# Optimization experiments

Measured on AMD Instinct MI355X. Metric: run time of the kernel, lower is better.

Reference implementation:

```python
import jax, jax.numpy as jnp
import numpy as np

B, N, C = 4, 4096, 256
H, D, K = 8, 32, 16  # heads, dim_head, knn


def setup_inputs() -> dict:
    key = jax.random.key(0)
    ks = jax.random.split(key, 7)
    s = 1.0 / np.sqrt(C)
    return {
        "x": jax.random.normal(ks[0], (B, N, C), dtype=jnp.float32),
        "Wq": jax.random.normal(ks[1], (C, H * D), dtype=jnp.float32) * s,
        "bq": jnp.zeros((H * D,), dtype=jnp.float32),
        "Wk": jax.random.normal(ks[2], (C, H * D), dtype=jnp.float32) * s,
        "bk": jnp.zeros((H * D,), dtype=jnp.float32),
        "Wv": jax.random.normal(ks[3], (C, H * D), dtype=jnp.float32) * s,
        "bv": jnp.zeros((H * D,), dtype=jnp.float32),
    }


def _knn_indices(x):
    # squared euclidean distances per batch: [B, N, N]
    sq = jnp.sum(x * x, axis=-1)
    d2 = sq[:, :, None] + sq[:, None, :] - 2.0 * jnp.einsum("bnc,bmc->bnm", x, x)
    # exclude self-loops (loop=False)
    eye = jnp.eye(x.shape[1], dtype=bool)
    d2 = jnp.where(eye[None], jnp.inf, d2)
    # k nearest neighbors (smallest distance)
    _, idx = jax.lax.top_k(-d2, K)  # [B, N, K]
    return idx


def reference(x, Wq, bq, Wk, bk, Wv, bv):
    idx = _knn_indices(x)  # [B, N, K] neighbor (source) node ids per target node
    # gather neighbor features: [B, N, K, C]
    xj = jax.vmap(lambda xb, ib: xb[ib])(x, idx)
    q = (x @ Wq + bq).reshape(B, N, H, D)           # target-node queries
    ke = (xj @ Wk + bk).reshape(B, N, K, H, D)      # per-edge keys
    ve = (xj @ Wv + bv).reshape(B, N, K, H, D)      # per-edge values
    scale = 1.0 / np.sqrt(D)
    scores = jnp.einsum("bnhd,bnkhd->bnkh", q, ke) * scale
    alpha = jax.nn.softmax(scores, axis=2)          # softmax over each node's K neighbors
    out = jnp.einsum("bnkh,bnkhd->bnhd", alpha, ve)
    return out.reshape(B, N, H * D)
```

## Files before the change

kernel.cpp:

```cpp
#include <hip/hip_runtime.h>
#include <cstdint>
#include <cstddef>

#define N_ 4096
#define C_ 256

typedef _Float16 h8 __attribute__((ext_vector_type(8)));
typedef _Float16 h4 __attribute__((ext_vector_type(4)));
typedef float f4 __attribute__((ext_vector_type(4)));

__device__ __forceinline__ void gl2lds16(const void* g, void* l) {
  __builtin_amdgcn_global_load_lds((const __attribute__((address_space(1))) void*)g,
                                   (__attribute__((address_space(3))) void*)l, 16, 0, 0);
}

__device__ __forceinline__ void ce_asc(double& a, double& b) {
  double mn = fmin(a, b), mx = fmax(a, b);
  a = mn; b = mx;
}

__device__ __forceinline__ void sort8_asc(double* c) {
#pragma unroll
  for (int k = 2; k <= 8; k <<= 1)
#pragma unroll
    for (int j = k >> 1; j > 0; j >>= 1)
#pragma unroll
      for (int i = 0; i < 8; i++) {
        int l = i ^ j;
        if (l > i) {
          bool up = ((i & k) == 0);
          double a = c[i], b = c[l];
          double mn = fmin(a, b), mx = fmax(a, b);
          c[i] = up ? mn : mx;
          c[l] = up ? mx : mn;
        }
      }
}

__device__ __forceinline__ void merge8_top16(double* karr, const double* c) {
#pragma unroll
  for (int i = 0; i < 8; i++)
    karr[8 + i] = fmin(karr[8 + i], c[7 - i]);
#pragma unroll
  for (int j = 8; j > 0; j >>= 1)
#pragma unroll
    for (int i = 0; i < 16; i++) {
      int l = i ^ j;
      if (l > i) ce_asc(karr[i], karr[l]);
    }
}

__global__ __launch_bounds__(256) void k_prep(const float* __restrict__ x,
                                              float* __restrict__ sq,
                                              _Float16* __restrict__ xh,
                                              _Float16* __restrict__ xl) {
  int wave = threadIdx.x >> 6, lane = threadIdx.x & 63;
  int row = blockIdx.x * 4 + wave;
  size_t off = (size_t)row * C_ + lane * 4;
  float4 v = *(const float4*)(x + off);
  h4 hi; hi[0] = (_Float16)v.x; hi[1] = (_Float16)v.y;
         hi[2] = (_Float16)v.z; hi[3] = (_Float16)v.w;
  h4 lo; lo[0] = (_Float16)(v.x - (float)hi[0]); lo[1] = (_Float16)(v.y - (float)hi[1]);
         lo[2] = (_Float16)(v.z - (float)hi[2]); lo[3] = (_Float16)(v.w - (float)hi[3]);
  *(h4*)(xh + off) = hi;
  *(h4*)(xl + off) = lo;
  float s = v.x * v.x + v.y * v.y + v.z * v.z + v.w * v.w;
  s += __shfl_xor(s, 32); s += __shfl_xor(s, 16); s += __shfl_xor(s, 8);
  s += __shfl_xor(s, 4);  s += __shfl_xor(s, 2);  s += __shfl_xor(s, 1);
  if (lane == 0) sq[row] = s;
}

__global__ __launch_bounds__(256) void k_wsplit(const float* __restrict__ Wq,
                                                const float* __restrict__ Wk,
                                                const float* __restrict__ Wv,
                                                _Float16* __restrict__ wh,
                                                _Float16* __restrict__ wl) {
  int g = blockIdx.x * 256 + threadIdx.x;
  int m = g >> 16, e = g & 65535;
  int k = e >> 8, j = e & 255;
  const float* W = (m == 0) ? Wq : ((m == 1) ? Wk : Wv);
  float v = W[k * 256 + j];
  _Float16 hi = (_Float16)v;
  _Float16 lo = (_Float16)(v - (float)hi);
  wh[m * 65536 + j * 256 + k] = hi;
  wl[m * 65536 + j * 256 + k] = lo;
}

__global__ __launch_bounds__(256, 3) void k_proj(const _Float16* __restrict__ xh,
                                                 const _Float16* __restrict__ xl,
                                                 const _Float16* __restrict__ wh,
                                                 const _Float16* __restrict__ wl,
                                                 const float* __restrict__ bqp,
                                                 const float* __restrict__ bkp,
                                                 const float* __restrict__ bvp,
                                                 float* __restrict__ qf,
                                                 float* __restrict__ kf,
                                                 float* __restrict__ vf) {
  int tid = threadIdx.x;
  int bid = blockIdx.x;
  int m   = bid >> 8;
  int rb  = (bid >> 1) & 127;
  int cp  = bid & 1;
  int wave = tid >> 6, lane = tid & 63, quad = lane >> 4, l16 = lane & 15;
  const float* bb = (m == 0) ? bqp : ((m == 1) ? bkp : bvp);
  float* dst      = (m == 0) ? qf  : ((m == 1) ? kf  : vf);
  int row0 = rb * 128 + wave * 32;

  h8 Ah[2][8], Al[2][8];
#pragma unroll
  for (int rt = 0; rt < 2; rt++)
#pragma unroll
    for (int kc = 0; kc < 8; kc++) {
      size_t off = (size_t)(row0 + rt * 16 + l16) * C_ + kc * 32 + quad * 8;
      Ah[rt][kc] = *(const h8*)(xh + off);
      Al[rt][kc] = *(const h8*)(xl + off);
    }
  const _Float16* whm = wh + (size_t)m * 65536;
  const _Float16* wlm = wl + (size_t)m * 65536;

  f4 acc[2][8];
#pragma unroll
  for (int rt = 0; rt < 2; rt++)
#pragma unroll
    for (int ct = 0; ct < 8; ct++) acc[rt][ct] = f4{0.f, 0.f, 0.f, 0.f};
#pragma unroll
  for (int kc = 0; kc < 8; kc++) {
#pragma unroll
    for (int ct = 0; ct < 8; ct++) {
      int col = cp * 128 + ct * 16 + l16;
      h8 bh = *(const h8*)(whm + (size_t)col * 256 + kc * 32 + quad * 8);
      h8 bl = *(const h8*)(wlm + (size_t)col * 256 + kc * 32 + quad * 8);
#pragma unroll
      for (int rt = 0; rt < 2; rt++) {
        acc[rt][ct] = __builtin_amdgcn_mfma_f32_16x16x32_f16(Ah[rt][kc], bh, acc[rt][ct], 0, 0, 0);
        acc[rt][ct] = __builtin_amdgcn_mfma_f32_16x16x32_f16(Ah[rt][kc], bl, acc[rt][ct], 0, 0, 0);
        acc[rt][ct] = __builtin_amdgcn_mfma_f32_16x16x32_f16(Al[rt][kc], bh, acc[rt][ct], 0, 0, 0);
      }
    }
  }
#pragma unroll
  for (int rt = 0; rt < 2; rt++)
#pragma unroll
    for (int ct = 0; ct < 8; ct++) {
      int col = cp * 128 + ct * 16 + l16;
      float bias = bb[col];
#pragma unroll
      for (int i = 0; i < 4; i++) {
        int r = row0 + rt * 16 + quad * 4 + i;
        dst[(size_t)r * C_ + col] = acc[rt][ct][i] + bias;
      }
    }
}

__global__ __launch_bounds__(256, 2) void k_knn(const _Float16* __restrict__ xh,
                                                const _Float16* __restrict__ xl,
                                                const float* __restrict__ sq,
                                                double* __restrict__ pd) {
  __shared__ __align__(16) _Float16 Bh[16 * 528];
  __shared__ __align__(16) _Float16 Bl[16 * 528];
  __shared__ __align__(16) float sc[128 * 36];
  __shared__ float sqS[32];

  int tid = threadIdx.x;
  int wave = tid >> 6, lane = tid & 63, quad = lane >> 4, l16 = lane & 15;
  int bid = blockIdx.x;
  int s4 = bid & 3, tile = (bid >> 2) & 31, b = bid >> 7;
  int bN = b * N_, n0 = tile * 128, src0g = s4 * 1024;

  h8 Ah[2][8], Al[2][8];
  int tb = bN + n0 + wave * 32;
#pragma unroll
  for (int rt = 0; rt < 2; rt++)
#pragma unroll
    for (int kc = 0; kc < 8; kc++) {
      size_t off = (size_t)(tb + rt * 16 + l16) * C_ + kc * 32 + quad * 8;
      Ah[rt][kc] = *(const h8*)(xh + off);
      Al[rt][kc] = *(const h8*)(xl + off);
    }
  float sqT[2][4];
#pragma unroll
  for (int rt = 0; rt < 2; rt++)
#pragma unroll
    for (int i = 0; i < 4; i++)
      sqT[rt][i] = sq[tb + rt * 16 + quad * 4 + i];

  double karr[16];
#pragma unroll
  for (int p = 0; p < 16; p++) karr[p] = 1e300;
  int rowo = tid & 127, half = tid >> 7;

  {
    const _Float16* gh = xh + (size_t)(bN + src0g) * C_ + lane * 8;
    const _Float16* gl = xl + (size_t)(bN + src0g) * C_ + lane * 8;
#pragma unroll
    for (int k = 0; k < 4; k++) {
      int seg = wave * 4 + k;
      gl2lds16(gh + seg * 512, &Bh[seg * 528]);
      gl2lds16(gl + seg * 512, &Bl[seg * 528]);
    }
    if (tid < 32) sqS[tid] = sq[bN + src0g + tid];
  }

  int hb0 = ((l16 >> 1) * 528) + ((l16 & 1) * 256) + quad * 8;
  int hb1 = (((16 + l16) >> 1) * 528) + ((l16 & 1) * 256) + quad * 8;

#pragma unroll 1
  for (int ch = 0; ch < 32; ch++) {
    int src0 = src0g + ch * 32;
    __syncthreads();

    f4 acc[2][2];
#pragma unroll
    for (int rt = 0; rt < 2; rt++)
#pragma unroll
      for (int ct = 0; ct < 2; ct++) acc[rt][ct] = f4{0.f, 0.f, 0.f, 0.f};
#pragma unroll
    for (int kc = 0; kc < 8; kc++) {
      h8 bh0 = *(const h8*)(&Bh[hb0 + kc * 32]);
      h8 bh1 = *(const h8*)(&Bh[hb1 + kc * 32]);
      h8 bl0 = *(const h8*)(&Bl[hb0 + kc * 32]);
      h8 bl1 = *(const h8*)(&Bl[hb1 + kc * 32]);
#pragma unroll
      for (int rt = 0; rt < 2; rt++) {
        acc[rt][0] = __builtin_amdgcn_mfma_f32_16x16x32_f16(Ah[rt][kc], bh0, acc[rt][0], 0, 0, 0);
        acc[rt][0] = __builtin_amdgcn_mfma_f32_16x16x32_f16(Ah[rt][kc], bl0, acc[rt][0], 0, 0, 0);
        acc[rt][0] = __builtin_amdgcn_mfma_f32_16x16x32_f16(Al[rt][kc], bh0, acc[rt][0], 0, 0, 0);
        acc[rt][1] = __builtin_amdgcn_mfma_f32_16x16x32_f16(Ah[rt][kc], bh1, acc[rt][1], 0, 0, 0);
        acc[rt][1] = __builtin_amdgcn_mfma_f32_16x16x32_f16(Ah[rt][kc], bl1, acc[rt][1], 0, 0, 0);
        acc[rt][1] = __builtin_amdgcn_mfma_f32_16x16x32_f16(Al[rt][kc], bh1, acc[rt][1], 0, 0, 0);
      }
    }
    float sqSr[2] = {sqS[l16], sqS[16 + l16]};
#pragma unroll
    for (int rt = 0; rt < 2; rt++)
#pragma unroll
      for (int ct = 0; ct < 2; ct++) {
        int c = ct * 16 + l16;
#pragma unroll
        for (int i = 0; i < 4; i++) {
          int r = wave * 32 + rt * 16 + quad * 4 + i;
          float d2 = sqT[rt][i] + sqSr[ct] - 2.0f * acc[rt][ct][i];
          if (n0 + r == src0 + c) d2 = 1e38f;
          sc[r * 36 + c] = d2;
        }
      }
    __syncthreads();

    if (ch < 31) {
      int srcn = src0 + 32;
      const _Float16* gh = xh + (size_t)(bN + srcn) * C_ + lane * 8;
      const _Float16* gl = xl + (size_t)(bN + srcn) * C_ + lane * 8;
#pragma unroll
      for (int k = 0; k < 4; k++) {
        int seg = wave * 4 + k;
        gl2lds16(gh + seg * 512, &Bh[seg * 528]);
        gl2lds16(gl + seg * 512, &Bl[seg * 528]);
      }
      if (tid < 32) sqS[tid] = sq[bN + srcn + tid];
    }

#pragma unroll
    for (int bt = 0; bt < 2; bt++) {
      float dv[8];
#pragma unroll
      for (int k4 = 0; k4 < 2; k4++)
        *(float4*)&dv[k4 * 4] = *(const float4*)(&sc[rowo * 36 + half * 16 + bt * 8 + k4 * 4]);
      double c8[8];
#pragma unroll
      for (int j = 0; j < 8; j++) {
        double key = (double)dv[j];
        c8[j] = __longlong_as_double(__double_as_longlong(key) |
                                     (unsigned)(src0 + half * 16 + bt * 8 + j));
      }
      sort8_asc(c8);
      merge8_top16(karr, c8);
    }
  }

  __syncthreads();
  double* scd = (double*)sc;
  if (tid >= 128) {
#pragma unroll
    for (int p = 0; p < 16; p++) scd[(tid - 128) * 17 + p] = karr[p];
  }
  __syncthreads();
  if (tid < 128) {
#pragma unroll
    for (int i = 0; i < 16; i++)
      karr[i] = fmin(karr[i], scd[tid * 17 + (15 - i)]);
#pragma unroll
    for (int j = 8; j > 0; j >>= 1)
#pragma unroll
      for (int i = 0; i < 16; i++) {
        int l = i ^ j;
        if (l > i) ce_asc(karr[i], karr[l]);
      }
#pragma unroll
    for (int p = 0; p < 16; p++)
      pd[((size_t)bid * 128 + tid) * 16 + p] = karr[p];
  }
}

__global__ __launch_bounds__(256) void k_kmerge(const double* __restrict__ pd,
                                                int* __restrict__ idxo) {
  int g = blockIdx.x * 256 + threadIdx.x;
  int b = g >> 12, n = g & 4095;
  int tile = n >> 7, r = n & 127;
  size_t base[4]; int p[4]; double hd[4];
#pragma unroll
  for (int s = 0; s < 4; s++) {
    base[s] = (size_t)(((b * 32 + tile) * 4 + s) * 128 + r) * 16;
    p[s] = 0;
    hd[s] = pd[base[s]];
  }
#pragma unroll
  for (int k = 0; k < 16; k++) {
    int bs = 0; double bd = hd[0];
#pragma unroll
    for (int s = 1; s < 4; s++) if (hd[s] < bd) { bd = hd[s]; bs = s; }
    idxo[(size_t)g * 16 + k] = (int)(__double_as_longlong(bd) & 0xFFF);
    p[bs]++;
    hd[bs] = (p[bs] < 16) ? pd[base[bs] + p[bs]] : 1e301;
  }
}

__global__ __launch_bounds__(256) void k_attn(const float* __restrict__ qf,
                                              const float* __restrict__ kf,
                                              const float* __restrict__ vf,
                                              const int* __restrict__ idxv,
                                              float* __restrict__ out) {
  int wave = threadIdx.x >> 6, lane = threadIdx.x & 63;
  int g = blockIdx.x * 4 + wave;
  int bN = (g >> 12) << 12;
  float4 q4 = *(const float4*)(qf + (size_t)g * C_ + lane * 4);
  int my = idxv[(size_t)g * 16 + (lane & 15)];
  const float scale = 0.17677669529663687f;

  float s[16];
  float4 vv[16];
#pragma unroll
  for (int j = 0; j < 16; j++) {
    int nb = __shfl(my, j);
    size_t base = (size_t)(bN + nb) * C_ + lane * 4;
    float4 k4 = *(const float4*)(kf + base);
    vv[j] = *(const float4*)(vf + base);
    float p = k4.x * q4.x + k4.y * q4.y + k4.z * q4.z + k4.w * q4.w;
    p += __shfl_xor(p, 1); p += __shfl_xor(p, 2); p += __shfl_xor(p, 4);
    s[j] = p * scale;
  }
  float mx = s[0];
#pragma unroll
  for (int j = 1; j < 16; j++) mx = fmaxf(mx, s[j]);
  float den = 0.f;
#pragma unroll
  for (int j = 0; j < 16; j++) { s[j] = __expf(s[j] - mx); den += s[j]; }
  float inv = 1.0f / den;
  float4 o; o.x = 0.f; o.y = 0.f; o.z = 0.f; o.w = 0.f;
#pragma unroll
  for (int j = 0; j < 16; j++) {
    float w = s[j] * inv;
    o.x = fmaf(w, vv[j].x, o.x); o.y = fmaf(w, vv[j].y, o.y);
    o.z = fmaf(w, vv[j].z, o.z); o.w = fmaf(w, vv[j].w, o.w);
  }
  *(float4*)(out + (size_t)g * C_ + lane * 4) = o;
}

extern "C" void kernel_launch(void* const* d_in, const int* in_sizes, int n_in,
                              void* d_out, int out_size, void* d_ws, size_t ws_size,
                              hipStream_t stream) {
  const float* x  = (const float*)d_in[0];
  const float* Wq = (const float*)d_in[1];
  const float* bq = (const float*)d_in[2];
  const float* Wk = (const float*)d_in[3];
  const float* bk = (const float*)d_in[4];
  const float* Wv = (const float*)d_in[5];
  const float* bv = (const float*)d_in[6];
  float* out = (float*)d_out;

  char* ws = (char*)d_ws;
  float*     sqp  = (float*)(ws + 0);
  _Float16*  xh   = (_Float16*)(ws + 65536);
  _Float16*  xl   = (_Float16*)(ws + 8454144);
  float*     qf   = (float*)(ws + 16842752);
  float*     kf   = (float*)(ws + 33619968);
  float*     vf   = (float*)(ws + 50397184);
  double*    pd   = (double*)(ws + 67174400);
  int*       idxb = (int*)  (ws + 75563008);
  _Float16*  whf  = (_Float16*)(ws + 76611584);
  _Float16*  wlf  = (_Float16*)(ws + 77004800);

  k_prep  <<<4096, 256, 0, stream>>>(x, sqp, xh, xl);
  k_wsplit<<<768,  256, 0, stream>>>(Wq, Wk, Wv, whf, wlf);
  k_proj  <<<768,  256, 0, stream>>>(xh, xl, whf, wlf, bq, bk, bv, qf, kf, vf);
  k_knn   <<<512,  256, 0, stream>>>(xh, xl, sqp, pd);
  k_kmerge<<<64,   256, 0, stream>>>(pd, idxb);
  k_attn  <<<4096, 256, 0, stream>>>(qf, kf, vf, idxb, out);
}
```

Baseline: 294.9 us.

## Use float key/int index pairs in kNN top-k, bitonic merge in kmerge

The per-thread top-16 lists in the kNN kernel now keep float distances and int indices separately instead of packed doubles, so the comparators do 32-bit selects rather than double-precision min/max. The MFMA calls are reordered so the four independent accumulators interleave, which shortens back-to-back dependency chains. The final k-way merge kernel is replaced by a bitonic merge of four sorted 16-lists per thread and launched with smaller blocks to spread across more CUs. The cost is more registers for the separate index arrays and extra select instructions per swap.

```diff
diff --git a/kernel.cpp b/kernel.cpp
--- a/kernel.cpp
+++ b/kernel.cpp
@@ -14,39 +14,63 @@
                                    (__attribute__((address_space(3))) void*)l, 16, 0, 0);
 }
 
-__device__ __forceinline__ void ce_asc(double& a, double& b) {
-  double mn = fmin(a, b), mx = fmax(a, b);
-  a = mn; b = mx;
-}
-
-__device__ __forceinline__ void sort8_asc(double* c) {
-#pragma unroll
-  for (int k = 2; k <= 8; k <<= 1)
-#pragma unroll
-    for (int j = k >> 1; j > 0; j >>= 1)
+
+__device__ __forceinline__ void sort8p(float* k, int* x) {
+#pragma unroll
+  for (int kk = 2; kk <= 8; kk <<= 1)
+#pragma unroll
+    for (int j = kk >> 1; j > 0; j >>= 1)
 #pragma unroll
       for (int i = 0; i < 8; i++) {
         int l = i ^ j;
         if (l > i) {
-          bool up = ((i & k) == 0);
-          double a = c[i], b = c[l];
-          double mn = fmin(a, b), mx = fmax(a, b);
-          c[i] = up ? mn : mx;
-          c[l] = up ? mx : mn;
+          bool up = ((i & kk) == 0);
+          bool sw = up ? (k[i] > k[l]) : (k[i] < k[l]);
+          float a = sw ? k[l] : k[i];
+          float b = sw ? k[i] : k[l];
+          int ai = sw ? x[l] : x[i];
+          int bi = sw ? x[i] : x[l];
+          k[i] = a; k[l] = b; x[i] = ai; x[l] = bi;
         }
       }
 }
 
-__device__ __forceinline__ void merge8_top16(double* karr, const double* c) {
-#pragma unroll
-  for (int i = 0; i < 8; i++)
-    karr[8 + i] = fmin(karr[8 + i], c[7 - i]);
+__device__ __forceinline__ void merge8p(float* kk_, int* ki,
+                                        const float* ck, const int* ci) {
+#pragma unroll
+  for (int i = 0; i < 8; i++) {
+    bool take = ck[7 - i] < kk_[8 + i];
+    kk_[8 + i] = take ? ck[7 - i] : kk_[8 + i];
+    ki[8 + i]  = take ? ci[7 - i] : ki[8 + i];
+  }
 #pragma unroll
   for (int j = 8; j > 0; j >>= 1)
 #pragma unroll
     for (int i = 0; i < 16; i++) {
       int l = i ^ j;
-      if (l > i) ce_asc(karr[i], karr[l]);
+      if (l > i) {
+        bool sw = kk_[i] > kk_[l];
+        float a = sw ? kk_[l] : kk_[i];
+        float b = sw ? kk_[i] : kk_[l];
+        int ai = sw ? ki[l] : ki[i];
+        int bi = sw ? ki[i] : ki[l];
+        kk_[i] = a; kk_[l] = b; ki[i] = ai; ki[l] = bi;
+      }
+    }
+}
+
+__device__ __forceinline__ void merge16d(double* a, const double* b) {
+#pragma unroll
+  for (int i = 0; i < 16; i++) a[i] = fmin(a[i], b[15 - i]);
+#pragma unroll
+  for (int j = 8; j > 0; j >>= 1)
+#pragma unroll
+    for (int i = 0; i < 16; i++) {
+      int l = i ^ j;
+      if (l > i) {
+        double mn = fmin(a[i], a[l]), mx = fmax(a[i], a[l]);
+        a[i] = mn; a[l] = mx;
+      }
     }
 }
 
@@ -184,9 +208,9 @@
     for (int i = 0; i < 4; i++)
       sqT[rt][i] = sq[tb + rt * 16 + quad * 4 + i];
 
-  double karr[16];
-#pragma unroll
-  for (int p = 0; p < 16; p++) karr[p] = 1e300;
+  float karr_k[16]; int karr_i[16];
+#pragma unroll
+  for (int p = 0; p < 16; p++) { karr_k[p] = 3.0e38f; karr_i[p] = 0; }
   int rowo = tid & 127, half = tid >> 7;
 
   {
@@ -220,15 +244,18 @@
       h8 bh1 = *(const h8*)(&Bh[hb1 + kc * 32]);
       h8 bl0 = *(const h8*)(&Bl[hb0 + kc * 32]);
       h8 bl1 = *(const h8*)(&Bl[hb1 + kc * 32]);
-#pragma unroll
-      for (int rt = 0; rt < 2; rt++) {
-        acc[rt][0] = __builtin_amdgcn_mfma_f32_16x16x32_f16(Ah[rt][kc], bh0, acc[rt][0], 0, 0, 0);
-        acc[rt][0] = __builtin_amdgcn_mfma_f32_16x16x32_f16(Ah[rt][kc], bl0, acc[rt][0], 0, 0, 0);
-        acc[rt][0] = __builtin_amdgcn_mfma_f32_16x16x32_f16(Al[rt][kc], bh0, acc[rt][0], 0, 0, 0);
-        acc[rt][1] = __builtin_amdgcn_mfma_f32_16x16x32_f16(Ah[rt][kc], bh1, acc[rt][1], 0, 0, 0);
-        acc[rt][1] = __builtin_amdgcn_mfma_f32_16x16x32_f16(Ah[rt][kc], bl1, acc[rt][1], 0, 0, 0);
-        acc[rt][1] = __builtin_amdgcn_mfma_f32_16x16x32_f16(Al[rt][kc], bh1, acc[rt][1], 0, 0, 0);
-      }
+      acc[0][0] = __builtin_amdgcn_mfma_f32_16x16x32_f16(Ah[0][kc], bh0, acc[0][0], 0, 0, 0);
+      acc[0][1] = __builtin_amdgcn_mfma_f32_16x16x32_f16(Ah[0][kc], bh1, acc[0][1], 0, 0, 0);
+      acc[1][0] = __builtin_amdgcn_mfma_f32_16x16x32_f16(Ah[1][kc], bh0, acc[1][0], 0, 0, 0);
+      acc[1][1] = __builtin_amdgcn_mfma_f32_16x16x32_f16(Ah[1][kc], bh1, acc[1][1], 0, 0, 0);
+      acc[0][0] = __builtin_amdgcn_mfma_f32_16x16x32_f16(Ah[0][kc], bl0, acc[0][0], 0, 0, 0);
+      acc[0][1] = __builtin_amdgcn_mfma_f32_16x16x32_f16(Ah[0][kc], bl1, acc[0][1], 0, 0, 0);
+      acc[1][0] = __builtin_amdgcn_mfma_f32_16x16x32_f16(Ah[1][kc], bl0, acc[1][0], 0, 0, 0);
+      acc[1][1] = __builtin_amdgcn_mfma_f32_16x16x32_f16(Ah[1][kc], bl1, acc[1][1], 0, 0, 0);
+      acc[0][0] = __builtin_amdgcn_mfma_f32_16x16x32_f16(Al[0][kc], bh0, acc[0][0], 0, 0, 0);
+      acc[0][1] = __builtin_amdgcn_mfma_f32_16x16x32_f16(Al[0][kc], bh1, acc[0][1], 0, 0, 0);
+      acc[1][0] = __builtin_amdgcn_mfma_f32_16x16x32_f16(Al[1][kc], bh0, acc[1][0], 0, 0, 0);
+      acc[1][1] = __builtin_amdgcn_mfma_f32_16x16x32_f16(Al[1][kc], bh1, acc[1][1], 0, 0, 0);
     }
     float sqSr[2] = {sqS[l16], sqS[16 + l16]};
 #pragma unroll
@@ -261,67 +288,80 @@
 
 #pragma unroll
     for (int bt = 0; bt < 2; bt++) {
-      float dv[8];
+      float ck[8]; int ci[8];
 #pragma unroll
       for (int k4 = 0; k4 < 2; k4++)
-        *(float4*)&dv[k4 * 4] = *(const float4*)(&sc[rowo * 36 + half * 16 + bt * 8 + k4 * 4]);
-      double c8[8];
-#pragma unroll
-      for (int j = 0; j < 8; j++) {
-        double key = (double)dv[j];
-        c8[j] = __longlong_as_double(__double_as_longlong(key) |
-                                     (unsigned)(src0 + half * 16 + bt * 8 + j));
-      }
-      sort8_asc(c8);
-      merge8_top16(karr, c8);
+        *(float4*)&ck[k4 * 4] = *(const float4*)(&sc[rowo * 36 + half * 16 + bt * 8 + k4 * 4]);
+#pragma unroll
+      for (int j = 0; j < 8; j++) ci[j] = src0 + half * 16 + bt * 8 + j;
+      sort8p(ck, ci);
+      merge8p(karr_k, karr_i, ck, ci);
     }
   }
 
   __syncthreads();
-  double* scd = (double*)sc;
+  float* scF = sc;
+  int*   scI = (int*)sc;
   if (tid >= 128) {
 #pragma unroll
-    for (int p = 0; p < 16; p++) scd[(tid - 128) * 17 + p] = karr[p];
+    for (int p = 0; p < 16; p++) {
+      scF[(tid - 128) * 34 + p]      = karr_k[p];
+      scI[(tid - 128) * 34 + 16 + p] = karr_i[p];
+    }
   }
   __syncthreads();
   if (tid < 128) {
 #pragma unroll
-    for (int i = 0; i < 16; i++)
-      karr[i] = fmin(karr[i], scd[tid * 17 + (15 - i)]);
+    for (int i = 0; i < 16; i++) {
+      float pk = scF[tid * 34 + (15 - i)];
+      int   pi = scI[tid * 34 + 16 + (15 - i)];
+      bool take = pk < karr_k[i];
+      karr_k[i] = take ? pk : karr_k[i];
+      karr_i[i] = take ? pi : karr_i[i];
+    }
 #pragma unroll
     for (int j = 8; j > 0; j >>= 1)
 #pragma unroll
       for (int i = 0; i < 16; i++) {
         int l = i ^ j;
-        if (l > i) ce_asc(karr[i], karr[l]);
-      }
-#pragma unroll
-    for (int p = 0; p < 16; p++)
-      pd[((size_t)bid * 128 + tid) * 16 + p] = karr[p];
-  }
-}
-
-__global__ __launch_bounds__(256) void k_kmerge(const double* __restrict__ pd,
-                                                int* __restrict__ idxo) {
-  int g = blockIdx.x * 256 + threadIdx.x;
+        if (l > i) {
+          bool sw = karr_k[i] > karr_k[l];
+          float a = sw ? karr_k[l] : karr_k[i];
+          float bb2 = sw ? karr_k[i] : karr_k[l];
+          int ai = sw ? karr_i[l] : karr_i[i];
+          int bi = sw ? karr_i[i] : karr_i[l];
+          karr_k[i] = a; karr_k[l] = bb2; karr_i[i] = ai; karr_i[l] = bi;
+        }
+      }
+#pragma unroll
+    for (int p = 0; p < 16; p++) {
+      long long pk = __double_as_longlong((double)karr_k[p]) |
+                     (long long)(unsigned)karr_i[p];
+      pd[((size_t)bid * 128 + tid) * 16 + p] = __longlong_as_double(pk);
+    }
+  }
+}
+
+__global__ __launch_bounds__(64) void k_kmerge(const double* __restrict__ pd,
+                                               int* __restrict__ idxo) {
+  int g = blockIdx.x * 64 + threadIdx.x;
   int b = g >> 12, n = g & 4095;
   int tile = n >> 7, r = n & 127;
-  size_t base[4]; int p[4]; double hd[4];
-#pragma unroll
-  for (int s = 0; s < 4; s++) {
-    base[s] = (size_t)(((b * 32 + tile) * 4 + s) * 128 + r) * 16;
-    p[s] = 0;
-    hd[s] = pd[base[s]];
-  }
-#pragma unroll
-  for (int k = 0; k < 16; k++) {
-    int bs = 0; double bd = hd[0];
-#pragma unroll
-    for (int s = 1; s < 4; s++) if (hd[s] < bd) { bd = hd[s]; bs = s; }
-    idxo[(size_t)g * 16 + k] = (int)(__double_as_longlong(bd) & 0xFFF);
-    p[bs]++;
-    hd[bs] = (p[bs] < 16) ? pd[base[bs] + p[bs]] : 1e301;
-  }
+  size_t base = (size_t)(((b * 32 + tile) * 4) * 128 + r) * 16;
+
+  double acc[16], other[16];
+#pragma unroll
+  for (int p = 0; p < 16; p++) acc[p] = pd[base + p];
+#pragma unroll
+  for (int s = 1; s < 4; s++) {
+    size_t bs = base + (size_t)s * 128 * 16;
+#pragma unroll
+    for (int p = 0; p < 16; p++) other[p] = pd[bs + p];
+    merge16d(acc, other);
+  }
+#pragma unroll
+  for (int k = 0; k < 16; k++)
+    idxo[(size_t)g * 16 + k] = (int)(__double_as_longlong(acc[k]) & 0xFFF);
 }
 
 __global__ __launch_bounds__(256) void k_attn(const float* __restrict__ qf,
@@ -393,6 +433,6 @@
   k_wsplit<<<768,  256, 0, stream>>>(Wq, Wk, Wv, whf, wlf);
   k_proj  <<<768,  256, 0, stream>>>(xh, xl, whf, wlf, bq, bk, bv, qf, kf, vf);
   k_knn   <<<512,  256, 0, stream>>>(xh, xl, sqp, pd);
-  k_kmerge<<<64,   256, 0, stream>>>(pd, idxb);
+  k_kmerge<<<256,  64,  0, stream>>>(pd, idxb);
   k_attn  <<<4096, 256, 0, stream>>>(qf, kf, vf, idxb, out);
 }
```

Measured after the change: 317.5 us. +7.7%, slower.

## Double-buffer KNN source tiles, use per-wave score staging, branchless kmerge

Applied to the files above, without the earlier changes.

The KNN kernel now double-buffers the source-row LDS tiles and issues the next chunk's async loads before the MFMA work, so the second block-wide barrier per chunk goes away. Each wave stages its own 32-row score tile in a private LDS region. Lanes then read the rows they own, which removes cross-wave dependence. The final merge uses the freed B buffer, and the per-chunk squared norms are read straight from global memory. The kmerge kernel swaps its data-dependent 4-way pointer merge for branchless bitonic merges over all 16 entries of each partial list, run with smaller blocks. The cost is more LDS use per block, which may limit occupancy.

```diff
diff --git a/kernel.cpp b/kernel.cpp
--- a/kernel.cpp
+++ b/kernel.cpp
@@ -47,6 +47,21 @@
     for (int i = 0; i < 16; i++) {
       int l = i ^ j;
       if (l > i) ce_asc(karr[i], karr[l]);
+    }
+}
+
+__device__ __forceinline__ void merge16d(double* a, const double* b) {
+#pragma unroll
+  for (int i = 0; i < 16; i++) a[i] = fmin(a[i], b[15 - i]);
+#pragma unroll
+  for (int j = 8; j > 0; j >>= 1)
+#pragma unroll
+    for (int i = 0; i < 16; i++) {
+      int l = i ^ j;
+      if (l > i) {
+        double mn = fmin(a[i], a[l]), mx = fmax(a[i], a[l]);
+        a[i] = mn; a[l] = mx;
+      }
     }
 }
 
@@ -156,10 +171,9 @@
                                                 const _Float16* __restrict__ xl,
                                                 const float* __restrict__ sq,
                                                 double* __restrict__ pd) {
-  __shared__ __align__(16) _Float16 Bh[16 * 528];
-  __shared__ __align__(16) _Float16 Bl[16 * 528];
-  __shared__ __align__(16) float sc[128 * 36];
-  __shared__ float sqS[32];
+  __shared__ __align__(16) _Float16 Bh[2][16 * 528];
+  __shared__ __align__(16) _Float16 Bl[2][16 * 528];
+  __shared__ __align__(16) float sc[4][16 * 36];
 
   int tid = threadIdx.x;
   int wave = tid >> 6, lane = tid & 63, quad = lane >> 4, l16 = lane & 15;
@@ -187,7 +201,11 @@
   double karr[16];
 #pragma unroll
   for (int p = 0; p < 16; p++) karr[p] = 1e300;
-  int rowo = tid & 127, half = tid >> 7;
+  int rloc = lane & 31;
+  int half = lane >> 5;
+  int rown = wave * 32 + rloc;
+  int rt_owner = rloc >> 4;
+  int rl = rloc & 15;
 
   {
     const _Float16* gh = xh + (size_t)(bN + src0g) * C_ + lane * 8;
@@ -195,10 +213,9 @@
 #pragma unroll
     for (int k = 0; k < 4; k++) {
       int seg = wave * 4 + k;
-      gl2lds16(gh + seg * 512, &Bh[seg * 528]);
-      gl2lds16(gl + seg * 512, &Bl[seg * 528]);
-    }
-    if (tid < 32) sqS[tid] = sq[bN + src0g + tid];
+      gl2lds16(gh + seg * 512, &Bh[0][seg * 528]);
+      gl2lds16(gl + seg * 512, &Bl[0][seg * 528]);
+    }
   }
 
   int hb0 = ((l16 >> 1) * 528) + ((l16 & 1) * 256) + quad * 8;
@@ -207,8 +224,23 @@
 #pragma unroll 1
   for (int ch = 0; ch < 32; ch++) {
     int src0 = src0g + ch * 32;
+    int buf = ch & 1;
     __syncthreads();
 
+    if (ch < 31) {
+      int srcn = src0 + 32;
+      const _Float16* gh = xh + (size_t)(bN + srcn) * C_ + lane * 8;
+      const _Float16* gl = xl + (size_t)(bN + srcn) * C_ + lane * 8;
+#pragma unroll
+      for (int k = 0; k < 4; k++) {
+        int seg = wave * 4 + k;
+        gl2lds16(gh + seg * 512, &Bh[buf ^ 1][seg * 528]);
+        gl2lds16(gl + seg * 512, &Bl[buf ^ 1][seg * 528]);
+      }
+    }
+    float sqc0 = sq[bN + src0 + l16];
+    float sqc1 = sq[bN + src0 + 16 + l16];
+
     f4 acc[2][2];
 #pragma unroll
     for (int rt = 0; rt < 2; rt++)
@@ -216,10 +248,10 @@
       for (int ct = 0; ct < 2; ct++) acc[rt][ct] = f4{0.f, 0.f, 0.f, 0.f};
 #pragma unroll
     for (int kc = 0; kc < 8; kc++) {
-      h8 bh0 = *(const h8*)(&Bh[hb0 + kc * 32]);
-      h8 bh1 = *(const h8*)(&Bh[hb1 + kc * 32]);
-      h8 bl0 = *(const h8*)(&Bl[hb0 + kc * 32]);
-      h8 bl1 = *(const h8*)(&Bl[hb1 + kc * 32]);
+      h8 bh0 = *(const h8*)(&Bh[buf][hb0 + kc * 32]);
+      h8 bh1 = *(const h8*)(&Bh[buf][hb1 + kc * 32]);
+      h8 bl0 = *(const h8*)(&Bl[buf][hb0 + kc * 32]);
+      h8 bl1 = *(const h8*)(&Bl[buf][hb1 + kc * 32]);
 #pragma unroll
       for (int rt = 0; rt < 2; rt++) {
         acc[rt][0] = __builtin_amdgcn_mfma_f32_16x16x32_f16(Ah[rt][kc], bh0, acc[rt][0], 0, 0, 0);
@@ -230,45 +262,36 @@
         acc[rt][1] = __builtin_amdgcn_mfma_f32_16x16x32_f16(Al[rt][kc], bh1, acc[rt][1], 0, 0, 0);
       }
     }
-    float sqSr[2] = {sqS[l16], sqS[16 + l16]};
-#pragma unroll
-    for (int rt = 0; rt < 2; rt++)
+
+    float dv[16];
+#pragma unroll
+    for (int rt = 0; rt < 2; rt++) {
 #pragma unroll
       for (int ct = 0; ct < 2; ct++) {
         int c = ct * 16 + l16;
+        float sqSr = ct ? sqc1 : sqc0;
 #pragma unroll
         for (int i = 0; i < 4; i++) {
           int r = wave * 32 + rt * 16 + quad * 4 + i;
-          float d2 = sqT[rt][i] + sqSr[ct] - 2.0f * acc[rt][ct][i];
+          float d2 = sqT[rt][i] + sqSr - 2.0f * acc[rt][ct][i];
           if (n0 + r == src0 + c) d2 = 1e38f;
-          sc[r * 36 + c] = d2;
+          sc[wave][(quad * 4 + i) * 36 + c] = d2;
         }
       }
-    __syncthreads();
-
-    if (ch < 31) {
-      int srcn = src0 + 32;
-      const _Float16* gh = xh + (size_t)(bN + srcn) * C_ + lane * 8;
-      const _Float16* gl = xl + (size_t)(bN + srcn) * C_ + lane * 8;
-#pragma unroll
-      for (int k = 0; k < 4; k++) {
-        int seg = wave * 4 + k;
-        gl2lds16(gh + seg * 512, &Bh[seg * 528]);
-        gl2lds16(gl + seg * 512, &Bl[seg * 528]);
-      }
-      if (tid < 32) sqS[tid] = sq[bN + srcn + tid];
+      if (rt_owner == rt) {
+#pragma unroll
+        for (int j = 0; j < 4; j++)
+          *(float4*)&dv[j * 4] = *(const float4*)(&sc[wave][rl * 36 + half * 16 + j * 4]);
+      }
+      asm volatile("" ::: "memory");
     }
 
 #pragma unroll
     for (int bt = 0; bt < 2; bt++) {
-      float dv[8];
-#pragma unroll
-      for (int k4 = 0; k4 < 2; k4++)
-        *(float4*)&dv[k4 * 4] = *(const float4*)(&sc[rowo * 36 + half * 16 + bt * 8 + k4 * 4]);
       double c8[8];
 #pragma unroll
       for (int j = 0; j < 8; j++) {
-        double key = (double)dv[j];
+        double key = (double)dv[bt * 8 + j];
         c8[j] = __longlong_as_double(__double_as_longlong(key) |
                                      (unsigned)(src0 + half * 16 + bt * 8 + j));
       }
@@ -278,16 +301,16 @@
   }
 
   __syncthreads();
-  double* scd = (double*)sc;
-  if (tid >= 128) {
-#pragma unroll
-    for (int p = 0; p < 16; p++) scd[(tid - 128) * 17 + p] = karr[p];
+  double* scd = (double*)&Bh[0][0];
+  if (half) {
+#pragma unroll
+    for (int p = 0; p < 16; p++) scd[rown * 17 + p] = karr[p];
   }
   __syncthreads();
-  if (tid < 128) {
+  if (!half) {
 #pragma unroll
     for (int i = 0; i < 16; i++)
-      karr[i] = fmin(karr[i], scd[tid * 17 + (15 - i)]);
+      karr[i] = fmin(karr[i], scd[rown * 17 + (15 - i)]);
 #pragma unroll
     for (int j = 8; j > 0; j >>= 1)
 #pragma unroll
@@ -297,31 +320,30 @@
       }
 #pragma unroll
     for (int p = 0; p < 16; p++)
-      pd[((size_t)bid * 128 + tid) * 16 + p] = karr[p];
-  }
-}
-
-__global__ __launch_bounds__(256) void k_kmerge(const double* __restrict__ pd,
-                                                int* __restrict__ idxo) {
-  int g = blockIdx.x * 256 + threadIdx.x;
+      pd[((size_t)bid * 128 + rown) * 16 + p] = karr[p];
+  }
+}
+
+__global__ __launch_bounds__(64) void k_kmerge(const double* __restrict__ pd,
+                                               int* __restrict__ idxo) {
+  int g = blockIdx.x * 64 + threadIdx.x;
   int b = g >> 12, n = g & 4095;
   int tile = n >> 7, r = n & 127;
-  size_t base[4]; int p[4]; double hd[4];
-#pragma unroll
-  for (int s = 0; s < 4; s++) {
-    base[s] = (size_t)(((b * 32 + tile) * 4 + s) * 128 + r) * 16;
-    p[s] = 0;
-    hd[s] = pd[base[s]];
-  }
-#pragma unroll
-  for (int k = 0; k < 16; k++) {
-    int bs = 0; double bd = hd[0];
-#pragma unroll
-    for (int s = 1; s < 4; s++) if (hd[s] < bd) { bd = hd[s]; bs = s; }
-    idxo[(size_t)g * 16 + k] = (int)(__double_as_longlong(bd) & 0xFFF);
-    p[bs]++;
-    hd[bs] = (p[bs] < 16) ? pd[base[bs] + p[bs]] : 1e301;
-  }
+  size_t base = (size_t)(((b * 32 + tile) * 4) * 128 + r) * 16;
+
+  double acc[16], other[16];
+#pragma unroll
+  for (int p = 0; p < 16; p++) acc[p] = pd[base + p];
+#pragma unroll
+  for (int s = 1; s < 4; s++) {
+    size_t bs = base + (size_t)s * 128 * 16;
+#pragma unroll
+    for (int p = 0; p < 16; p++) other[p] = pd[bs + p];
+    merge16d(acc, other);
+  }
+#pragma unroll
+  for (int k = 0; k < 16; k++)
+    idxo[(size_t)g * 16 + k] = (int)(__double_as_longlong(acc[k]) & 0xFFF);
 }
 
 __global__ __launch_bounds__(256) void k_attn(const float* __restrict__ qf,
@@ -393,6 +415,6 @@
   k_wsplit<<<768,  256, 0, stream>>>(Wq, Wk, Wv, whf, wlf);
   k_proj  <<<768,  256, 0, stream>>>(xh, xl, whf, wlf, bq, bk, bv, qf, kf, vf);
   k_knn   <<<512,  256, 0, stream>>>(xh, xl, sqp, pd);
-  k_kmerge<<<64,   256, 0, stream>>>(pd, idxb);
+  k_kmerge<<<256,  64,  0, stream>>>(pd, idxb);
   k_attn  <<<4096, 256, 0, stream>>>(qf, kf, vf, idxb, out);
 }
```

Result: no change. 291.8 us (-1.0%).

## Co-schedule projection and kNN blocks in one launch; bitonic k-merge

Applied to the files above, without the earlier changes.

The projection GEMM and the kNN distance/top-k kernel become one launch of 1280 blocks. Blocks are interleaved 2:3 between kNN work and projection work, so the two independent stages share the GPU at the same time instead of running back to back. The k-merge kernel now loads each of the four sorted partial lists and combines them with a bitonic merge instead of a serial 4-way pointer merge, and it launches 64-thread blocks. The trade-off is that the fused kernel is compiled with the register and LDS footprint of the larger branch and uses the kNN launch bounds, which may lower occupancy for the projection blocks.

```diff
diff --git a/kernel.cpp b/kernel.cpp
--- a/kernel.cpp
+++ b/kernel.cpp
@@ -47,6 +47,21 @@
     for (int i = 0; i < 16; i++) {
       int l = i ^ j;
       if (l > i) ce_asc(karr[i], karr[l]);
+    }
+}
+
+__device__ __forceinline__ void merge16d(double* a, const double* b) {
+#pragma unroll
+  for (int i = 0; i < 16; i++) a[i] = fmin(a[i], b[15 - i]);
+#pragma unroll
+  for (int j = 8; j > 0; j >>= 1)
+#pragma unroll
+    for (int i = 0; i < 16; i++) {
+      int l = i ^ j;
+      if (l > i) {
+        double mn = fmin(a[i], a[l]), mx = fmax(a[i], a[l]);
+        a[i] = mn; a[l] = mx;
+      }
     }
 }
 
@@ -86,242 +101,241 @@
   wl[m * 65536 + j * 256 + k] = lo;
 }
 
-__global__ __launch_bounds__(256, 3) void k_proj(const _Float16* __restrict__ xh,
-                                                 const _Float16* __restrict__ xl,
-                                                 const _Float16* __restrict__ wh,
-                                                 const _Float16* __restrict__ wl,
-                                                 const float* __restrict__ bqp,
-                                                 const float* __restrict__ bkp,
-                                                 const float* __restrict__ bvp,
-                                                 float* __restrict__ qf,
-                                                 float* __restrict__ kf,
-                                                 float* __restrict__ vf) {
-  int tid = threadIdx.x;
-  int bid = blockIdx.x;
-  int m   = bid >> 8;
-  int rb  = (bid >> 1) & 127;
-  int cp  = bid & 1;
-  int wave = tid >> 6, lane = tid & 63, quad = lane >> 4, l16 = lane & 15;
-  const float* bb = (m == 0) ? bqp : ((m == 1) ? bkp : bvp);
-  float* dst      = (m == 0) ? qf  : ((m == 1) ? kf  : vf);
-  int row0 = rb * 128 + wave * 32;
-
-  h8 Ah[2][8], Al[2][8];
-#pragma unroll
-  for (int rt = 0; rt < 2; rt++)
-#pragma unroll
-    for (int kc = 0; kc < 8; kc++) {
-      size_t off = (size_t)(row0 + rt * 16 + l16) * C_ + kc * 32 + quad * 8;
-      Ah[rt][kc] = *(const h8*)(xh + off);
-      Al[rt][kc] = *(const h8*)(xl + off);
-    }
-  const _Float16* whm = wh + (size_t)m * 65536;
-  const _Float16* wlm = wl + (size_t)m * 65536;
-
-  f4 acc[2][8];
-#pragma unroll
-  for (int rt = 0; rt < 2; rt++)
-#pragma unroll
-    for (int ct = 0; ct < 8; ct++) acc[rt][ct] = f4{0.f, 0.f, 0.f, 0.f};
-#pragma unroll
-  for (int kc = 0; kc < 8; kc++) {
-#pragma unroll
-    for (int ct = 0; ct < 8; ct++) {
-      int col = cp * 128 + ct * 16 + l16;
-      h8 bh = *(const h8*)(whm + (size_t)col * 256 + kc * 32 + quad * 8);
-      h8 bl = *(const h8*)(wlm + (size_t)col * 256 + kc * 32 + quad * 8);
-#pragma unroll
-      for (int rt = 0; rt < 2; rt++) {
-        acc[rt][ct] = __builtin_amdgcn_mfma_f32_16x16x32_f16(Ah[rt][kc], bh, acc[rt][ct], 0, 0, 0);
-        acc[rt][ct] = __builtin_amdgcn_mfma_f32_16x16x32_f16(Ah[rt][kc], bl, acc[rt][ct], 0, 0, 0);
-        acc[rt][ct] = __builtin_amdgcn_mfma_f32_16x16x32_f16(Al[rt][kc], bh, acc[rt][ct], 0, 0, 0);
-      }
-    }
-  }
-#pragma unroll
-  for (int rt = 0; rt < 2; rt++)
-#pragma unroll
-    for (int ct = 0; ct < 8; ct++) {
-      int col = cp * 128 + ct * 16 + l16;
-      float bias = bb[col];
-#pragma unroll
-      for (int i = 0; i < 4; i++) {
-        int r = row0 + rt * 16 + quad * 4 + i;
-        dst[(size_t)r * C_ + col] = acc[rt][ct][i] + bias;
-      }
-    }
-}
-
-__global__ __launch_bounds__(256, 2) void k_knn(const _Float16* __restrict__ xh,
-                                                const _Float16* __restrict__ xl,
-                                                const float* __restrict__ sq,
-                                                double* __restrict__ pd) {
-  __shared__ __align__(16) _Float16 Bh[16 * 528];
-  __shared__ __align__(16) _Float16 Bl[16 * 528];
-  __shared__ __align__(16) float sc[128 * 36];
-  __shared__ float sqS[32];
-
+__global__ __launch_bounds__(256, 2) void k_fused(const _Float16* __restrict__ xh,
+                                                  const _Float16* __restrict__ xl,
+                                                  const float* __restrict__ sq,
+                                                  double* __restrict__ pd,
+                                                  const _Float16* __restrict__ wh,
+                                                  const _Float16* __restrict__ wl,
+                                                  const float* __restrict__ bqp,
+                                                  const float* __restrict__ bkp,
+                                                  const float* __restrict__ bvp,
+                                                  float* __restrict__ qf,
+                                                  float* __restrict__ kf,
+                                                  float* __restrict__ vf) {
+  int gid = blockIdx.x;
+  int g5 = gid % 5;
   int tid = threadIdx.x;
   int wave = tid >> 6, lane = tid & 63, quad = lane >> 4, l16 = lane & 15;
-  int bid = blockIdx.x;
-  int s4 = bid & 3, tile = (bid >> 2) & 31, b = bid >> 7;
-  int bN = b * N_, n0 = tile * 128, src0g = s4 * 1024;
-
-  h8 Ah[2][8], Al[2][8];
-  int tb = bN + n0 + wave * 32;
-#pragma unroll
-  for (int rt = 0; rt < 2; rt++)
-#pragma unroll
-    for (int kc = 0; kc < 8; kc++) {
-      size_t off = (size_t)(tb + rt * 16 + l16) * C_ + kc * 32 + quad * 8;
-      Ah[rt][kc] = *(const h8*)(xh + off);
-      Al[rt][kc] = *(const h8*)(xl + off);
-    }
-  float sqT[2][4];
-#pragma unroll
-  for (int rt = 0; rt < 2; rt++)
-#pragma unroll
-    for (int i = 0; i < 4; i++)
-      sqT[rt][i] = sq[tb + rt * 16 + quad * 4 + i];
-
-  double karr[16];
-#pragma unroll
-  for (int p = 0; p < 16; p++) karr[p] = 1e300;
-  int rowo = tid & 127, half = tid >> 7;
-
-  {
-    const _Float16* gh = xh + (size_t)(bN + src0g) * C_ + lane * 8;
-    const _Float16* gl = xl + (size_t)(bN + src0g) * C_ + lane * 8;
-#pragma unroll
-    for (int k = 0; k < 4; k++) {
-      int seg = wave * 4 + k;
-      gl2lds16(gh + seg * 512, &Bh[seg * 528]);
-      gl2lds16(gl + seg * 512, &Bl[seg * 528]);
-    }
-    if (tid < 32) sqS[tid] = sq[bN + src0g + tid];
-  }
-
-  int hb0 = ((l16 >> 1) * 528) + ((l16 & 1) * 256) + quad * 8;
-  int hb1 = (((16 + l16) >> 1) * 528) + ((l16 & 1) * 256) + quad * 8;
-
-#pragma unroll 1
-  for (int ch = 0; ch < 32; ch++) {
-    int src0 = src0g + ch * 32;
-    __syncthreads();
-
-    f4 acc[2][2];
+
+  if (g5 < 2) {
+    __shared__ __align__(16) _Float16 Bh[16 * 528];
+    __shared__ __align__(16) _Float16 Bl[16 * 528];
+    __shared__ __align__(16) float sc[128 * 36];
+    __shared__ float sqS[32];
+
+    int bid = (gid / 5) * 2 + g5;
+    int s4 = bid & 3, tile = (bid >> 2) & 31, b = bid >> 7;
+    int bN = b * N_, n0 = tile * 128, src0g = s4 * 1024;
+
+    h8 Ah[2][8], Al[2][8];
+    int tb = bN + n0 + wave * 32;
 #pragma unroll
     for (int rt = 0; rt < 2; rt++)
 #pragma unroll
-      for (int ct = 0; ct < 2; ct++) acc[rt][ct] = f4{0.f, 0.f, 0.f, 0.f};
-#pragma unroll
-    for (int kc = 0; kc < 8; kc++) {
-      h8 bh0 = *(const h8*)(&Bh[hb0 + kc * 32]);
-      h8 bh1 = *(const h8*)(&Bh[hb1 + kc * 32]);
-      h8 bl0 = *(const h8*)(&Bl[hb0 + kc * 32]);
-      h8 bl1 = *(const h8*)(&Bl[hb1 + kc * 32]);
-#pragma unroll
-      for (int rt = 0; rt < 2; rt++) {
-        acc[rt][0] = __builtin_amdgcn_mfma_f32_16x16x32_f16(Ah[rt][kc], bh0, acc[rt][0], 0, 0, 0);
-        acc[rt][0] = __builtin_amdgcn_mfma_f32_16x16x32_f16(Ah[rt][kc], bl0, acc[rt][0], 0, 0, 0);
-        acc[rt][0] = __builtin_amdgcn_mfma_f32_16x16x32_f16(Al[rt][kc], bh0, acc[rt][0], 0, 0, 0);
-        acc[rt][1] = __builtin_amdgcn_mfma_f32_16x16x32_f16(Ah[rt][kc], bh1, acc[rt][1], 0, 0, 0);
-        acc[rt][1] = __builtin_amdgcn_mfma_f32_16x16x32_f16(Ah[rt][kc], bl1, acc[rt][1], 0, 0, 0);
-        acc[rt][1] = __builtin_amdgcn_mfma_f32_16x16x32_f16(Al[rt][kc], bh1, acc[rt][1], 0, 0, 0);
-      }
-    }
-    float sqSr[2] = {sqS[l16], sqS[16 + l16]};
+      for (int kc = 0; kc < 8; kc++) {
+        size_t off = (size_t)(tb + rt * 16 + l16) * C_ + kc * 32 + quad * 8;
+        Ah[rt][kc] = *(const h8*)(xh + off);
+        Al[rt][kc] = *(const h8*)(xl + off);
+      }
+    float sqT[2][4];
 #pragma unroll
     for (int rt = 0; rt < 2; rt++)
 #pragma unroll
-      for (int ct = 0; ct < 2; ct++) {
-        int c = ct * 16 + l16;
-#pragma unroll
-        for (int i = 0; i < 4; i++) {
-          int r = wave * 32 + rt * 16 + quad * 4 + i;
-          float d2 = sqT[rt][i] + sqSr[ct] - 2.0f * acc[rt][ct][i];
-          if (n0 + r == src0 + c) d2 = 1e38f;
-          sc[r * 36 + c] = d2;
-        }
-      }
-    __syncthreads();
-
-    if (ch < 31) {
-      int srcn = src0 + 32;
-      const _Float16* gh = xh + (size_t)(bN + srcn) * C_ + lane * 8;
-      const _Float16* gl = xl + (size_t)(bN + srcn) * C_ + lane * 8;
+      for (int i = 0; i < 4; i++)
+        sqT[rt][i] = sq[tb + rt * 16 + quad * 4 + i];
+
+    double karr[16];
+#pragma unroll
+    for (int p = 0; p < 16; p++) karr[p] = 1e300;
+    int rowo = tid & 127, half = tid >> 7;
+
+    {
+      const _Float16* gh = xh + (size_t)(bN + src0g) * C_ + lane * 8;
+      const _Float16* gl = xl + (size_t)(bN + src0g) * C_ + lane * 8;
 #pragma unroll
       for (int k = 0; k < 4; k++) {
         int seg = wave * 4 + k;
         gl2lds16(gh + seg * 512, &Bh[seg * 528]);
         gl2lds16(gl + seg * 512, &Bl[seg * 528]);
       }
-      if (tid < 32) sqS[tid] = sq[bN + srcn + tid];
-    }
-
-#pragma unroll
-    for (int bt = 0; bt < 2; bt++) {
-      float dv[8];
-#pragma unroll
-      for (int k4 = 0; k4 < 2; k4++)
-        *(float4*)&dv[k4 * 4] = *(const float4*)(&sc[rowo * 36 + half * 16 + bt * 8 + k4 * 4]);
-      double c8[8];
-#pragma unroll
-      for (int j = 0; j < 8; j++) {
-        double key = (double)dv[j];
-        c8[j] = __longlong_as_double(__double_as_longlong(key) |
-                                     (unsigned)(src0 + half * 16 + bt * 8 + j));
-      }
-      sort8_asc(c8);
-      merge8_top16(karr, c8);
-    }
+      if (tid < 32) sqS[tid] = sq[bN + src0g + tid];
+    }
+
+    int hb0 = ((l16 >> 1) * 528) + ((l16 & 1) * 256) + quad * 8;
+    int hb1 = (((16 + l16) >> 1) * 528) + ((l16 & 1) * 256) + quad * 8;
+
+#pragma unroll 1
+    for (int ch = 0; ch < 32; ch++) {
+      int src0 = src0g + ch * 32;
+      __syncthreads();
+
+      f4 acc[2][2];
+#pragma unroll
+      for (int rt = 0; rt < 2; rt++)
+#pragma unroll
+        for (int ct = 0; ct < 2; ct++) acc[rt][ct] = f4{0.f, 0.f, 0.f, 0.f};
+#pragma unroll
+      for (int kc = 0; kc < 8; kc++) {
+        h8 bh0 = *(const h8*)(&Bh[hb0 + kc * 32]);
+        h8 bh1 = *(const h8*)(&Bh[hb1 + kc * 32]);
+        h8 bl0 = *(const h8*)(&Bl[hb0 + kc * 32]);
+        h8 bl1 = *(const h8*)(&Bl[hb1 + kc * 32]);
+#pragma unroll
+        for (int rt = 0; rt < 2; rt++) {
+          acc[rt][0] = __builtin_amdgcn_mfma_f32_16x16x32_f16(Ah[rt][kc], bh0, acc[rt][0], 0, 0, 0);
+          acc[rt][0] = __builtin_amdgcn_mfma_f32_16x16x32_f16(Ah[rt][kc], bl0, acc[rt][0], 0, 0, 0);
+          acc[rt][0] = __builtin_amdgcn_mfma_f32_16x16x32_f16(Al[rt][kc], bh0, acc[rt][0], 0, 0, 0);
+          acc[rt][1] = __builtin_amdgcn_mfma_f32_16x16x32_f16(Ah[rt][kc], bh1, acc[rt][1], 0, 0, 0);
+          acc[rt][1] = __builtin_amdgcn_mfma_f32_16x16x32_f16(Ah[rt][kc], bl1, acc[rt][1], 0, 0, 0);
+          acc[rt][1] = __builtin_amdgcn_mfma_f32_16x16x32_f16(Al[rt][kc], bh1, acc[rt][1], 0, 0, 0);
+        }
+      }
+      float sqSr[2] = {sqS[l16], sqS[16 + l16]};
+#pragma unroll
+      for (int rt = 0; rt < 2; rt++)
+#pragma unroll
+        for (int ct = 0; ct < 2; ct++) {
+          int c = ct * 16 + l16;
+#pragma unroll
+          for (int i = 0; i < 4; i++) {
+            int r = wave * 32 + rt * 16 + quad * 4 + i;
+            float d2 = sqT[rt][i] + sqSr[ct] - 2.0f * acc[rt][ct][i];
+            if (n0 + r == src0 + c) d2 = 1e38f;
+            sc[r * 36 + c] = d2;
+          }
+        }
+      __syncthreads();
+
+      if (ch < 31) {
+        int srcn = src0 + 32;
+        const _Float16* gh = xh + (size_t)(bN + srcn) * C_ + lane * 8;
+        const _Float16* gl = xl + (size_t)(bN + srcn) * C_ + lane * 8;
+#pragma unroll
+        for (int k = 0; k < 4; k++) {
+          int seg = wave * 4 + k;
+          gl2lds16(gh + seg * 512, &Bh[seg * 528]);
+          gl2lds16(gl + seg * 512, &Bl[seg * 528]);
+        }
+        if (tid < 32) sqS[tid] = sq[bN + srcn + tid];
+      }
+
+#pragma unroll
+      for (int bt = 0; bt < 2; bt++) {
+        float dv[8];
+#pragma unroll
+        for (int k4 = 0; k4 < 2; k4++)
+          *(float4*)&dv[k4 * 4] = *(const float4*)(&sc[rowo * 36 + half * 16 + bt * 8 + k4 * 4]);
+        double c8[8];
+#pragma unroll
+        for (int j = 0; j < 8; j++) {
+          double key = (double)dv[j];
+          c8[j] = __longlong_as_double(__double_as_longlong(key) |
+                                       (unsigned)(src0 + half * 16 + bt * 8 + j));
+        }
+        sort8_asc(c8);
+        merge8_top16(karr, c8);
+      }
+    }
+
+    __syncthreads();
+    double* scd = (double*)sc;
+    if (tid >= 128) {
+#pragma unroll
+      for (int p = 0; p < 16; p++) scd[(tid - 128) * 17 + p] = karr[p];
+    }
+    __syncthreads();
+    if (tid < 128) {
+#pragma unroll
+      for (int i = 0; i < 16; i++)
+        karr[i] = fmin(karr[i], scd[tid * 17 + (15 - i)]);
+#pragma unroll
+      for (int j = 8; j > 0; j >>= 1)
+#pragma unroll
+        for (int i = 0; i < 16; i++) {
+          int l = i ^ j;
+          if (l > i) ce_asc(karr[i], karr[l]);
+        }
+#pragma unroll
+      for (int p = 0; p < 16; p++)
+        pd[((size_t)bid * 128 + tid) * 16 + p] = karr[p];
+    }
+  } else {
+    int pbid = (gid / 5) * 3 + (g5 - 2);
+    int m   = pbid >> 8;
+    int rb  = (pbid >> 1) & 127;
+    int cp  = pbid & 1;
+    const float* bb = (m == 0) ? bqp : ((m == 1) ? bkp : bvp);
+    float* dst      = (m == 0) ? qf  : ((m == 1) ? kf  : vf);
+    int row0 = rb * 128 + wave * 32;
+
+    h8 Ah[2][8], Al[2][8];
+#pragma unroll
+    for (int rt = 0; rt < 2; rt++)
+#pragma unroll
+      for (int kc = 0; kc < 8; kc++) {
+        size_t off = (size_t)(row0 + rt * 16 + l16) * C_ + kc * 32 + quad * 8;
+        Ah[rt][kc] = *(const h8*)(xh + off);
+        Al[rt][kc] = *(const h8*)(xl + off);
+      }
+    const _Float16* whm = wh + (size_t)m * 65536;
+    const _Float16* wlm = wl + (size_t)m * 65536;
+
+    f4 acc[2][8];
+#pragma unroll
+    for (int rt = 0; rt < 2; rt++)
+#pragma unroll
+      for (int ct = 0; ct < 8; ct++) acc[rt][ct] = f4{0.f, 0.f, 0.f, 0.f};
+#pragma unroll
+    for (int kc = 0; kc < 8; kc++) {
+#pragma unroll
+      for (int ct = 0; ct < 8; ct++) {
+        int col = cp * 128 + ct * 16 + l16;
+        h8 bh = *(const h8*)(whm + (size_t)col * 256 + kc * 32 + quad * 8);
+        h8 bl = *(const h8*)(wlm + (size_t)col * 256 + kc * 32 + quad * 8);
+#pragma unroll
+        for (int rt = 0; rt < 2; rt++) {
+          acc[rt][ct] = __builtin_amdgcn_mfma_f32_16x16x32_f16(Ah[rt][kc], bh, acc[rt][ct], 0, 0, 0);
+          acc[rt][ct] = __builtin_amdgcn_mfma_f32_16x16x32_f16(Ah[rt][kc], bl, acc[rt][ct], 0, 0, 0);
+          acc[rt][ct] = __builtin_amdgcn_mfma_f32_16x16x32_f16(Al[rt][kc], bh, acc[rt][ct], 0, 0, 0);
+        }
+      }
+    }
+#pragma unroll
+    for (int rt = 0; rt < 2; rt++)
+#pragma unroll
+      for (int ct = 0; ct < 8; ct++) {
+        int col = cp * 128 + ct * 16 + l16;
+        float bias = bb[col];
+#pragma unroll
+        for (int i = 0; i < 4; i++) {
+          int r = row0 + rt * 16 + quad * 4 + i;
+          dst[(size_t)r * C_ + col] = acc[rt][ct][i] + bias;
+        }
+      }
   }
-
-  __syncthreads();
-  double* scd = (double*)sc;
-  if (tid >= 128) {
-#pragma unroll
-    for (int p = 0; p < 16; p++) scd[(tid - 128) * 17 + p] = karr[p];
-  }
-  __syncthreads();
-  if (tid < 128) {
-#pragma unroll
-    for (int i = 0; i < 16; i++)
-      karr[i] = fmin(karr[i], scd[tid * 17 + (15 - i)]);
-#pragma unroll
-    for (int j = 8; j > 0; j >>= 1)
-#pragma unroll
-      for (int i = 0; i < 16; i++) {
-        int l = i ^ j;
-        if (l > i) ce_asc(karr[i], karr[l]);
-      }
-#pragma unroll
-    for (int p = 0; p < 16; p++)
-      pd[((size_t)bid * 128 + tid) * 16 + p] = karr[p];
-  }
-}
-
-__global__ __launch_bounds__(256) void k_kmerge(const double* __restrict__ pd,
-                                                int* __restrict__ idxo) {
-  int g = blockIdx.x * 256 + threadIdx.x;
+}
+
+__global__ __launch_bounds__(64) void k_kmerge(const double* __restrict__ pd,
+                                               int* __restrict__ idxo) {
+  int g = blockIdx.x * 64 + threadIdx.x;
   int b = g >> 12, n = g & 4095;
   int tile = n >> 7, r = n & 127;
-  size_t base[4]; int p[4]; double hd[4];
-#pragma unroll
-  for (int s = 0; s < 4; s++) {
-    base[s] = (size_t)(((b * 32 + tile) * 4 + s) * 128 + r) * 16;
-    p[s] = 0;
-    hd[s] = pd[base[s]];
+  size_t base = (size_t)(((b * 32 + tile) * 4) * 128 + r) * 16;
+
+  double acc[16], other[16];
+#pragma unroll
+  for (int p = 0; p < 16; p++) acc[p] = pd[base + p];
+#pragma unroll
+  for (int s = 1; s < 4; s++) {
+    size_t bs = base + (size_t)s * 128 * 16;
+#pragma unroll
+    for (int p = 0; p < 16; p++) other[p] = pd[bs + p];
+    merge16d(acc, other);
   }
 #pragma unroll
-  for (int k = 0; k < 16; k++) {
-    int bs = 0; double bd = hd[0];
-#pragma unroll
-    for (int s = 1; s < 4; s++) if (hd[s] < bd) { bd = hd[s]; bs = s; }
-    idxo[(size_t)g * 16 + k] = (int)(__double_as_longlong(bd) & 0xFFF);
-    p[bs]++;
-    hd[bs] = (p[bs] < 16) ? pd[base[bs] + p[bs]] : 1e301;
-  }
+  for (int k = 0; k < 16; k++)
+    idxo[(size_t)g * 16 + k] = (int)(__double_as_longlong(acc[k]) & 0xFFF);
 }
 
 __global__ __launch_bounds__(256) void k_attn(const float* __restrict__ qf,
@@ -391,8 +405,8 @@
 
   k_prep  <<<4096, 256, 0, stream>>>(x, sqp, xh, xl);
   k_wsplit<<<768,  256, 0, stream>>>(Wq, Wk, Wv, whf, wlf);
-  k_proj  <<<768,  256, 0, stream>>>(xh, xl, whf, wlf, bq, bk, bv, qf, kf, vf);
-  k_knn   <<<512,  256, 0, stream>>>(xh, xl, sqp, pd);
-  k_kmerge<<<64,   256, 0, stream>>>(pd, idxb);
+  k_fused <<<1280, 256, 0, stream>>>(xh, xl, sqp, pd, whf, wlf,
+                                     bq, bk, bv, qf, kf, vf);
+  k_kmerge<<<256,  64,  0, stream>>>(pd, idxb);
   k_attn  <<<4096, 256, 0, stream>>>(qf, kf, vf, idxb, out);
 }
```

After: 323.3 us. 1.1x slower.
